# Kernel tuning notes

Measured on AMD Instinct MI355X. Metric: run time of the kernel, lower is better.

Reference implementation:

```python
import jax, jax.numpy as jnp
import numpy as np


def setup_inputs() -> dict:
    key = jax.random.key(0)
    k1, k2, k3 = jax.random.split(key, 3)
    B, T, S, D = 8, 2048, 2048, 512
    main_input = jax.random.normal(k1, (B, T, D), dtype=jnp.float32)
    attn_input = jax.random.normal(k2, (B, S, D), dtype=jnp.float32)
    # f_input is a torch Linear(D, D): y = x @ W_f.T + b_f
    W_f = jax.random.normal(k3, (D, D), dtype=jnp.float32) * (1.0 / np.sqrt(D))
    b_f = jnp.zeros((D,), dtype=jnp.float32)
    return {"main_input": main_input, "attn_input": attn_input, "W_f": W_f, "b_f": b_f}


def reference(main_input, attn_input, W_f, b_f):
    # keys: f_input applied to each attn word  [B,S,D]
    keys = jnp.einsum("bsd,ed->bse", attn_input, W_f) + b_f
    # scores[b,t,s] = keys[b,s,:] . main_input[b,t,:]
    scores = jnp.einsum("bse,bte->bts", keys, main_input)
    attn = jax.nn.softmax(scores, axis=-1)  # softmax over attn words S
    # weighted sum of RAW attn_input (values are unprojected)
    out = jnp.einsum("bts,bsd->btd", attn, attn_input)
    return out
```

## Files before the change

kernel.cpp:

```cpp
#include <hip/hip_runtime.h>
#include <math.h>

#define B_  8
#define T_  2048
#define S_  2048
#define D_  512

typedef _Float16 half8   __attribute__((ext_vector_type(8)));
typedef _Float16 half4_t __attribute__((ext_vector_type(4)));
typedef float    floatx4 __attribute__((ext_vector_type(4)));

__device__ __forceinline__ floatx4 mfma16(half8 a, half8 b, floatx4 c) {
  return __builtin_amdgcn_mfma_f32_16x16x32_f16(a, b, c, 0, 0, 0);
}

__device__ __forceinline__ void async16(void* lds, const void* g) {
  __builtin_amdgcn_global_load_lds(
      (const __attribute__((address_space(1))) void*)g,
      (__attribute__((address_space(3))) void*)lds, 16, 0, 0);
}

__device__ __forceinline__ void bar_lds() {
  __builtin_amdgcn_sched_barrier(0);
  asm volatile("s_waitcnt lgkmcnt(0)" ::: "memory");
  __builtin_amdgcn_s_barrier();
  __builtin_amdgcn_sched_barrier(0);
}

__global__ __launch_bounds__(256) void transpose_cast_kernel(
    const float* __restrict__ attn, _Float16* __restrict__ Vt) {
  __shared__ _Float16 tile[32][33];
  const int tx = threadIdx.x, ty = threadIdx.y;
  const int b = blockIdx.z, s0 = blockIdx.y * 32, d0 = blockIdx.x * 32;
  const float* src = attn + ((size_t)b * S_ + s0) * D_ + d0;
#pragma unroll
  for (int i = 0; i < 4; ++i) {
    int s = ty + i * 8;
    tile[tx][s] = (_Float16)src[(size_t)s * D_ + tx];
  }
  __syncthreads();
  _Float16* dst = Vt + ((size_t)b * D_ + d0) * S_ + s0;
#pragma unroll
  for (int i = 0; i < 4; ++i) {
    int d = ty + i * 8;
    dst[(size_t)d * S_ + tx] = tile[d][tx];
  }
}

__global__ __launch_bounds__(512, 2) void keys_gemm_kernel(
    const float* __restrict__ X, const float* __restrict__ W,
    const float* __restrict__ bias, _Float16* __restrict__ K16) {
  __shared__ alignas(16) _Float16 Xs[128][72];
  __shared__ alignas(16) _Float16 Ws[128][72];
  const int t = threadIdx.x;
  const int wave = t >> 6, lane = t & 63, q = lane >> 4, n = lane & 15;
  const int wm = wave >> 2, wn = wave & 3;
  const int m0 = blockIdx.x * 128, n0 = blockIdx.y * 128;

  floatx4 acc[4][2];
#pragma unroll
  for (int i = 0; i < 4; ++i)
#pragma unroll
    for (int j = 0; j < 2; ++j) {
      floatx4 z = {0.f, 0.f, 0.f, 0.f};
      acc[i][j] = z;
    }

  for (int kc = 0; kc < 8; ++kc) {
    const int k0 = kc * 64;
#pragma unroll
    for (int i = 0; i < 4; ++i) {
      int seg = i * 512 + t;
      int row = seg >> 4, c4 = (seg & 15) * 4;
      floatx4 xv = *(const floatx4*)&X[(size_t)(m0 + row) * D_ + k0 + c4];
      floatx4 wv = *(const floatx4*)&W[(size_t)(n0 + row) * D_ + k0 + c4];
      half4_t xh, wh;
#pragma unroll
      for (int j = 0; j < 4; ++j) { xh[j] = (_Float16)xv[j]; wh[j] = (_Float16)wv[j]; }
      *(half4_t*)&Xs[row][c4] = xh;
      *(half4_t*)&Ws[row][c4] = wh;
    }
    __syncthreads();
#pragma unroll
    for (int kk = 0; kk < 2; ++kk) {
      half8 a[4], bb[2];
#pragma unroll
      for (int mt = 0; mt < 4; ++mt)
        a[mt] = *(const half8*)&Xs[wm * 64 + mt * 16 + n][kk * 32 + q * 8];
#pragma unroll
      for (int nt = 0; nt < 2; ++nt)
        bb[nt] = *(const half8*)&Ws[wn * 32 + nt * 16 + n][kk * 32 + q * 8];
#pragma unroll
      for (int mt = 0; mt < 4; ++mt)
#pragma unroll
        for (int nt = 0; nt < 2; ++nt)
          acc[mt][nt] = mfma16(a[mt], bb[nt], acc[mt][nt]);
    }
    __syncthreads();
  }

#pragma unroll
  for (int nt = 0; nt < 2; ++nt) {
    int col = n0 + wn * 32 + nt * 16 + n;
    float bv = bias[col];
#pragma unroll
    for (int mt = 0; mt < 4; ++mt)
#pragma unroll
      for (int r = 0; r < 4; ++r) {
        int row = m0 + wm * 64 + mt * 16 + q * 4 + r;
        K16[(size_t)row * D_ + col] = (_Float16)(acc[mt][nt][r] + bv);
      }
  }
}

__global__ __launch_bounds__(512, 2) void flash_kernel(
    const float* __restrict__ Qf, const _Float16* __restrict__ K16,
    const _Float16* __restrict__ Vt, float* __restrict__ out) {
  __shared__ alignas(16) _Float16 Klds[2][32][512];
  __shared__ alignas(16) _Float16 Vlds[2][512][32];
  __shared__ alignas(16) _Float16 Pscr[4][16][40];
  __shared__ float Mscr[4][2][16];

  const int t = threadIdx.x;
  const int w = t >> 6, lane = t & 63, qd = lane >> 4, n = lane & 15;
  const int n7 = n & 7;
  const int rg = w >> 1, h = w & 1;
  const int bid = blockIdx.x;
  const int b = bid & 7, t0 = (bid >> 3) * 64;

  const _Float16* Kb = K16 + (size_t)b * S_ * D_;
  const _Float16* Vb = Vt + (size_t)b * D_ * S_;

  const int vsw = (lane & 3) ^ ((lane >> 3) & 3);
  const int ccV = qd ^ ((n >> 1) & 3);

  half8 qreg[16];
  {
    const float* qrow = Qf + ((size_t)b * T_ + t0 + rg * 16 + n) * D_;
#pragma unroll
    for (int kk = 0; kk < 16; ++kk) {
      floatx4 v0 = *(const floatx4*)&qrow[kk * 32 + qd * 8];
      floatx4 v1 = *(const floatx4*)&qrow[kk * 32 + qd * 8 + 4];
      half8 hv;
#pragma unroll
      for (int j = 0; j < 4; ++j) { hv[j] = (_Float16)v0[j]; hv[j + 4] = (_Float16)v1[j]; }
      qreg[kk] = hv;
    }
  }

  floatx4 O[17];
#pragma unroll
  for (int ng = 0; ng < 17; ++ng) {
    floatx4 z = {0.f, 0.f, 0.f, 0.f};
    O[ng] = z;
  }
  float m_st[4];
#pragma unroll
  for (int r = 0; r < 4; ++r) m_st[r] = -1e30f;

  half8 ones8;
#pragma unroll
  for (int j = 0; j < 8; ++j) ones8[j] = (_Float16)1.0f;

#pragma unroll
  for (int i = 0; i < 4; ++i) {
    int row = w * 4 + i;
    async16(&Klds[0][row][0], Kb + (size_t)row * D_ + ((lane ^ (row & 7)) * 8));
  }
#pragma unroll
  for (int i = 0; i < 4; ++i) {
    int d0 = (w * 4 + i) * 16;
    async16(&Vlds[0][d0][0], Vb + (size_t)(d0 + (lane >> 2)) * S_ + vsw * 8);
  }
  __syncthreads();

  for (int st = 0; st < S_ / 32; ++st) {
    const int cur = st & 1, nxt = cur ^ 1;
    const int s0 = st * 32;

    if (st < S_ / 32 - 1) {
#pragma unroll
      for (int i = 0; i < 4; ++i) {
        int row = w * 4 + i;
        async16(&Klds[nxt][row][0],
                Kb + (size_t)(s0 + 32 + row) * D_ + ((lane ^ (row & 7)) * 8));
      }
#pragma unroll
      for (int i = 0; i < 4; ++i) {
        int d0 = (w * 4 + i) * 16;
        async16(&Vlds[nxt][d0][0],
                Vb + (size_t)(d0 + (lane >> 2)) * S_ + s0 + 32 + vsw * 8);
      }
    }

    floatx4 Sa = {0.f, 0.f, 0.f, 0.f}, Sb = Sa;
#pragma unroll
    for (int kk = 0; kk < 8; ++kk) {
      int slot = (kk * 4 + qd) ^ n7;
      half8 bk = *(const half8*)&Klds[cur][h * 16 + n][slot * 8];
      Sa = mfma16(qreg[kk], bk, Sa);
    }
#pragma unroll
    for (int kk = 8; kk < 16; ++kk) {
      int slot = (kk * 4 + qd) ^ n7;
      half8 bk = *(const half8*)&Klds[cur][h * 16 + n][slot * 8];
      Sb = mfma16(qreg[kk], bk, Sb);
    }
    floatx4 Sc = Sa + Sb;

#pragma unroll
    for (int r = 0; r < 4; ++r) {
      float v = Sc[r];
      v = fmaxf(v, __shfl_xor(v, 1, 16));
      v = fmaxf(v, __shfl_xor(v, 2, 16));
      v = fmaxf(v, __shfl_xor(v, 4, 16));
      v = fmaxf(v, __shfl_xor(v, 8, 16));
      if (n == qd * 4 + r) Mscr[rg][h][n] = v;
    }
    bar_lds();

    float alpha[4];
#pragma unroll
    for (int r = 0; r < 4; ++r) {
      int row = qd * 4 + r;
      float mt = fmaxf(Mscr[rg][0][row], Mscr[rg][1][row]);
      float mn = fmaxf(m_st[r], mt);
      alpha[r] = __expf(m_st[r] - mn);
      m_st[r] = mn;
    }
    bool unchanged = (alpha[0] == 1.f) & (alpha[1] == 1.f) &
                     (alpha[2] == 1.f) & (alpha[3] == 1.f);
    if (!__all(unchanged)) {
#pragma unroll
      for (int ng = 0; ng < 17; ++ng)
#pragma unroll
        for (int r = 0; r < 4; ++r) O[ng][r] *= alpha[r];
    }

#pragma unroll
    for (int r = 0; r < 4; ++r) {
      float p = __expf(Sc[r] - m_st[r]);
      Pscr[rg][qd * 4 + r][h * 16 + n] = (_Float16)p;
    }
    bar_lds();

    half8 av = *(const half8*)&Pscr[rg][n][qd * 8];

#pragma unroll
    for (int ng = 0; ng < 16; ++ng) {
      half8 bv = *(const half8*)&Vlds[cur][h * 256 + ng * 16 + n][ccV * 8];
      O[ng] = mfma16(av, bv, O[ng]);
    }
    O[16] = mfma16(av, ones8, O[16]);

    if (st < S_ / 32 - 1) __syncthreads();
  }

  float* ob = out + ((size_t)b * T_ + t0 + rg * 16) * D_ + h * 256;
#pragma unroll
  for (int r = 0; r < 4; ++r) {
    float inv = 1.f / O[16][r];
    const size_t rowoff = (size_t)(qd * 4 + r) * D_;
#pragma unroll
    for (int ng = 0; ng < 16; ++ng)
      ob[rowoff + ng * 16 + n] = O[ng][r] * inv;
  }
}

extern "C" void kernel_launch(void* const* d_in, const int* in_sizes, int n_in,
                              void* d_out, int out_size, void* d_ws, size_t ws_size,
                              hipStream_t stream) {
  (void)in_sizes; (void)n_in; (void)out_size; (void)ws_size;
  const float* main_in = (const float*)d_in[0];
  const float* attn_in = (const float*)d_in[1];
  const float* W_f     = (const float*)d_in[2];
  const float* b_f     = (const float*)d_in[3];
  float* out = (float*)d_out;

  _Float16* K16 = (_Float16*)d_ws;
  _Float16* Vt  = K16 + (size_t)B_ * S_ * D_;

  transpose_cast_kernel<<<dim3(D_ / 32, S_ / 32, B_), dim3(32, 8, 1), 0, stream>>>(
      attn_in, Vt);
  keys_gemm_kernel<<<dim3((B_ * S_) / 128, D_ / 128), 512, 0, stream>>>(
      attn_in, W_f, b_f, K16);
  flash_kernel<<<(B_ * T_) / 64, 512, 0, stream>>>(main_in, K16, Vt, out);
}
```

Measured before the change: 293.5 us.

## Split KV tile across wave pair to drop per-step max exchange barriers

Each wave in a pair now owns half of every 32-wide S tile and keeps its own independent running max and sum over the full D=512 output, using 16x16x16 MFMAs on its 16 keys. This removes the two LDS barriers per step that were used to share row maxima and P between the two waves. The partial results are merged once at the end through shared memory. The cost is double the O accumulator registers (33 floatx4 instead of 17), which risks register spills or lower occupancy under launch_bounds(512,2), and twice as many narrower MFMAs for P·V.

```diff
diff --git a/kernel.cpp b/kernel.cpp
--- a/kernel.cpp
+++ b/kernel.cpp
@@ -13,18 +13,14 @@
 __device__ __forceinline__ floatx4 mfma16(half8 a, half8 b, floatx4 c) {
   return __builtin_amdgcn_mfma_f32_16x16x32_f16(a, b, c, 0, 0, 0);
 }
+__device__ __forceinline__ floatx4 mfma16k16(half4_t a, half4_t b, floatx4 c) {
+  return __builtin_amdgcn_mfma_f32_16x16x16f16(a, b, c, 0, 0, 0);
+}
 
 __device__ __forceinline__ void async16(void* lds, const void* g) {
   __builtin_amdgcn_global_load_lds(
       (const __attribute__((address_space(1))) void*)g,
       (__attribute__((address_space(3))) void*)lds, 16, 0, 0);
-}
-
-__device__ __forceinline__ void bar_lds() {
-  __builtin_amdgcn_sched_barrier(0);
-  asm volatile("s_waitcnt lgkmcnt(0)" ::: "memory");
-  __builtin_amdgcn_s_barrier();
-  __builtin_amdgcn_sched_barrier(0);
 }
 
 __global__ __launch_bounds__(256) void transpose_cast_kernel(
@@ -116,10 +112,11 @@
 __global__ __launch_bounds__(512, 2) void flash_kernel(
     const float* __restrict__ Qf, const _Float16* __restrict__ K16,
     const _Float16* __restrict__ Vt, float* __restrict__ out) {
-  __shared__ alignas(16) _Float16 Klds[2][32][512];
-  __shared__ alignas(16) _Float16 Vlds[2][512][32];
-  __shared__ alignas(16) _Float16 Pscr[4][16][40];
-  __shared__ float Mscr[4][2][16];
+  __shared__ alignas(16) unsigned char smem[137728];
+  _Float16* Kl = (_Float16*)smem;
+  _Float16* Vl = (_Float16*)(smem + 65536);
+  _Float16* Pp = (_Float16*)(smem + 131072);
+  float*    Mm = (float*)(smem + 137216);
 
   const int t = threadIdx.x;
   const int w = t >> 6, lane = t & 63, qd = lane >> 4, n = lane & 15;
@@ -132,7 +129,7 @@
   const _Float16* Vb = Vt + (size_t)b * D_ * S_;
 
   const int vsw = (lane & 3) ^ ((lane >> 3) & 3);
-  const int ccV = qd ^ ((n >> 1) & 3);
+  const int voff = (((h * 2 + (qd >> 1)) ^ ((n >> 1) & 3)) * 8) + (qd & 1) * 4;
 
   half8 qreg[16];
   {
@@ -148,9 +145,9 @@
     }
   }
 
-  floatx4 O[17];
-#pragma unroll
-  for (int ng = 0; ng < 17; ++ng) {
+  floatx4 O[33];
+#pragma unroll
+  for (int ng = 0; ng < 33; ++ng) {
     floatx4 z = {0.f, 0.f, 0.f, 0.f};
     O[ng] = z;
   }
@@ -158,19 +155,19 @@
 #pragma unroll
   for (int r = 0; r < 4; ++r) m_st[r] = -1e30f;
 
-  half8 ones8;
-#pragma unroll
-  for (int j = 0; j < 8; ++j) ones8[j] = (_Float16)1.0f;
+  half4_t ones4;
+#pragma unroll
+  for (int j = 0; j < 4; ++j) ones4[j] = (_Float16)1.0f;
 
 #pragma unroll
   for (int i = 0; i < 4; ++i) {
     int row = w * 4 + i;
-    async16(&Klds[0][row][0], Kb + (size_t)row * D_ + ((lane ^ (row & 7)) * 8));
+    async16(Kl + (size_t)row * 512, Kb + (size_t)row * D_ + ((lane ^ (row & 7)) * 8));
   }
 #pragma unroll
   for (int i = 0; i < 4; ++i) {
     int d0 = (w * 4 + i) * 16;
-    async16(&Vlds[0][d0][0], Vb + (size_t)(d0 + (lane >> 2)) * S_ + vsw * 8);
+    async16(Vl + (size_t)d0 * 32, Vb + (size_t)(d0 + (lane >> 2)) * S_ + vsw * 8);
   }
   __syncthreads();
 
@@ -182,32 +179,32 @@
 #pragma unroll
       for (int i = 0; i < 4; ++i) {
         int row = w * 4 + i;
-        async16(&Klds[nxt][row][0],
+        async16(Kl + ((size_t)nxt * 32 + row) * 512,
                 Kb + (size_t)(s0 + 32 + row) * D_ + ((lane ^ (row & 7)) * 8));
       }
 #pragma unroll
       for (int i = 0; i < 4; ++i) {
         int d0 = (w * 4 + i) * 16;
-        async16(&Vlds[nxt][d0][0],
+        async16(Vl + ((size_t)nxt * 512 + d0) * 32,
                 Vb + (size_t)(d0 + (lane >> 2)) * S_ + s0 + 32 + vsw * 8);
       }
     }
 
+    const _Float16* krow = Kl + ((size_t)cur * 32 + h * 16 + n) * 512;
     floatx4 Sa = {0.f, 0.f, 0.f, 0.f}, Sb = Sa;
 #pragma unroll
     for (int kk = 0; kk < 8; ++kk) {
       int slot = (kk * 4 + qd) ^ n7;
-      half8 bk = *(const half8*)&Klds[cur][h * 16 + n][slot * 8];
-      Sa = mfma16(qreg[kk], bk, Sa);
+      Sa = mfma16(qreg[kk], *(const half8*)&krow[slot * 8], Sa);
     }
 #pragma unroll
     for (int kk = 8; kk < 16; ++kk) {
       int slot = (kk * 4 + qd) ^ n7;
-      half8 bk = *(const half8*)&Klds[cur][h * 16 + n][slot * 8];
-      Sb = mfma16(qreg[kk], bk, Sb);
+      Sb = mfma16(qreg[kk], *(const half8*)&krow[slot * 8], Sb);
     }
     floatx4 Sc = Sa + Sb;
 
+    float alpha[4];
 #pragma unroll
     for (int r = 0; r < 4; ++r) {
       float v = Sc[r];
@@ -215,16 +212,7 @@
       v = fmaxf(v, __shfl_xor(v, 2, 16));
       v = fmaxf(v, __shfl_xor(v, 4, 16));
       v = fmaxf(v, __shfl_xor(v, 8, 16));
-      if (n == qd * 4 + r) Mscr[rg][h][n] = v;
-    }
-    bar_lds();
-
-    float alpha[4];
-#pragma unroll
-    for (int r = 0; r < 4; ++r) {
-      int row = qd * 4 + r;
-      float mt = fmaxf(Mscr[rg][0][row], Mscr[rg][1][row]);
-      float mn = fmaxf(m_st[r], mt);
+      float mn = fmaxf(m_st[r], v);
       alpha[r] = __expf(m_st[r] - mn);
       m_st[r] = mn;
     }
@@ -232,7 +220,7 @@
                      (alpha[2] == 1.f) & (alpha[3] == 1.f);
     if (!__all(unchanged)) {
 #pragma unroll
-      for (int ng = 0; ng < 17; ++ng)
+      for (int ng = 0; ng < 33; ++ng)
 #pragma unroll
         for (int r = 0; r < 4; ++r) O[ng][r] *= alpha[r];
     }
@@ -240,30 +228,64 @@
 #pragma unroll
     for (int r = 0; r < 4; ++r) {
       float p = __expf(Sc[r] - m_st[r]);
-      Pscr[rg][qd * 4 + r][h * 16 + n] = (_Float16)p;
-    }
-    bar_lds();
-
-    half8 av = *(const half8*)&Pscr[rg][n][qd * 8];
-
-#pragma unroll
-    for (int ng = 0; ng < 16; ++ng) {
-      half8 bv = *(const half8*)&Vlds[cur][h * 256 + ng * 16 + n][ccV * 8];
-      O[ng] = mfma16(av, bv, O[ng]);
-    }
-    O[16] = mfma16(av, ones8, O[16]);
+      Pp[((size_t)w * 16 + qd * 4 + r) * 24 + n] = (_Float16)p;
+    }
+    half4_t av = *(const half4_t*)&Pp[((size_t)w * 16 + n) * 24 + qd * 4];
+
+    const _Float16* vbase = Vl + (size_t)cur * 512 * 32;
+#pragma unroll
+    for (int ng = 0; ng < 32; ++ng) {
+      half4_t bv = *(const half4_t*)&vbase[(size_t)(ng * 16 + n) * 32 + voff];
+      O[ng] = mfma16k16(av, bv, O[ng]);
+    }
+    O[32] = mfma16k16(av, ones4, O[32]);
 
     if (st < S_ / 32 - 1) __syncthreads();
   }
 
-  float* ob = out + ((size_t)b * T_ + t0 + rg * 16) * D_ + h * 256;
+  if (n == 0) {
+#pragma unroll
+    for (int r = 0; r < 4; ++r) Mm[w * 16 + qd * 4 + r] = m_st[r];
+  }
+  __syncthreads();
+
+  float fac[4], lp[4];
 #pragma unroll
   for (int r = 0; r < 4; ++r) {
-    float inv = 1.f / O[16][r];
-    const size_t rowoff = (size_t)(qd * 4 + r) * D_;
-#pragma unroll
-    for (int ng = 0; ng < 16; ++ng)
-      ob[rowoff + ng * 16 + n] = O[ng][r] * inv;
+    float mo = Mm[(w ^ 1) * 16 + qd * 4 + r];
+    float mn = fmaxf(m_st[r], mo);
+    fac[r] = __expf(m_st[r] - mn);
+    lp[r] = O[32][r] * fac[r];
+  }
+
+  float* Ob = (float*)smem;
+  float* Lb = (float*)(smem + 131072);
+  if (h == 1) {
+#pragma unroll
+    for (int ng = 0; ng < 32; ++ng)
+#pragma unroll
+      for (int r = 0; r < 4; ++r)
+        Ob[(size_t)(rg * 16 + qd * 4 + r) * 512 + ng * 16 + n] = O[ng][r] * fac[r];
+    if (n == 0) {
+#pragma unroll
+      for (int r = 0; r < 4; ++r) Lb[rg * 16 + qd * 4 + r] = lp[r];
+    }
+  }
+  __syncthreads();
+
+  if (h == 0) {
+    float* ob = out + ((size_t)b * T_ + t0 + rg * 16) * D_;
+#pragma unroll
+    for (int r = 0; r < 4; ++r) {
+      float lt = lp[r] + Lb[rg * 16 + qd * 4 + r];
+      float inv = 1.f / lt;
+      const size_t rowoff = (size_t)(qd * 4 + r) * D_;
+#pragma unroll
+      for (int ng = 0; ng < 32; ++ng)
+        ob[rowoff + ng * 16 + n] =
+            (O[ng][r] * fac[r] +
+             Ob[(size_t)(rg * 16 + qd * 4 + r) * 512 + ng * 16 + n]) * inv;
+    }
   }
 }
 
```

Result: slower. 381.2 us (+29.9%).

## Precompute LDS/global byte offsets, interleave QK MFMAs, lazy softmax rescale, set priority

Applied to the files above, without the earlier changes.

Replaces per-iteration index arithmetic for the K/V async loads and LDS fragment reads with precomputed byte pointers and incremented offsets. It interleaves the two QK accumulator chains and wraps the MFMA loops in s_setprio to favour matrix issue. The online-softmax rescale now runs only when a row max grows by more than 8 (lazy rescaling). This lets exp values exceed 1 by up to e^8 in fp16, which adds some overflow and precision risk. The goal is fewer VALU/SALU instructions and skipped O rescales.

```diff
diff --git a/kernel.cpp b/kernel.cpp
--- a/kernel.cpp
+++ b/kernel.cpp
@@ -128,11 +128,29 @@
   const int bid = blockIdx.x;
   const int b = bid & 7, t0 = (bid >> 3) * 64;
 
-  const _Float16* Kb = K16 + (size_t)b * S_ * D_;
-  const _Float16* Vb = Vt + (size_t)b * D_ * S_;
+  const char* Kb = (const char*)(K16 + (size_t)b * S_ * D_);
+  const char* Vb = (const char*)(Vt + (size_t)b * D_ * S_);
 
   const int vsw = (lane & 3) ^ ((lane >> 3) & 3);
   const int ccV = qd ^ ((n >> 1) & 3);
+
+  const int ks = n7 >> 2;
+  const int kq = (qd ^ (n7 & 3)) * 16;
+  const int krow_b = (h * 16 + n) * 1024;
+  const char* KL = (const char*)Klds;
+  const char* kbe0 = KL + krow_b + kq + ks * 64;
+  const char* kbo0 = KL + krow_b + kq + 64 - ks * 64;
+  const char* VL = (const char*)Vlds;
+  const char* vb0 = VL + h * 16384 + n * 64 + ccV * 16;
+  const _Float16* prd = &Pscr[rg][n][qd * 8];
+
+  unsigned int koff[4], voff[4];
+#pragma unroll
+  for (int i = 0; i < 4; ++i) {
+    int row = w * 4 + i;
+    koff[i] = (unsigned int)((row * 512 + (lane ^ (row & 7)) * 8) * 2);
+    voff[i] = (unsigned int)(((row * 16 + (lane >> 2)) * S_ + vsw * 8) * 2);
+  }
 
   half8 qreg[16];
   {
@@ -165,47 +183,37 @@
 #pragma unroll
   for (int i = 0; i < 4; ++i) {
     int row = w * 4 + i;
-    async16(&Klds[0][row][0], Kb + (size_t)row * D_ + ((lane ^ (row & 7)) * 8));
-  }
-#pragma unroll
-  for (int i = 0; i < 4; ++i) {
-    int d0 = (w * 4 + i) * 16;
-    async16(&Vlds[0][d0][0], Vb + (size_t)(d0 + (lane >> 2)) * S_ + vsw * 8);
+    async16(&Klds[0][row][0], Kb + koff[i]);
+    async16(&Vlds[0][row * 16][0], Vb + voff[i]);
+    koff[i] += 32768;
+    voff[i] += 64;
   }
   __syncthreads();
 
   for (int st = 0; st < S_ / 32; ++st) {
     const int cur = st & 1, nxt = cur ^ 1;
-    const int s0 = st * 32;
 
     if (st < S_ / 32 - 1) {
 #pragma unroll
       for (int i = 0; i < 4; ++i) {
         int row = w * 4 + i;
-        async16(&Klds[nxt][row][0],
-                Kb + (size_t)(s0 + 32 + row) * D_ + ((lane ^ (row & 7)) * 8));
+        async16(&Klds[nxt][row][0], Kb + koff[i]);
+        async16(&Vlds[nxt][row * 16][0], Vb + voff[i]);
+        koff[i] += 32768;
+        voff[i] += 64;
       }
-#pragma unroll
-      for (int i = 0; i < 4; ++i) {
-        int d0 = (w * 4 + i) * 16;
-        async16(&Vlds[nxt][d0][0],
-                Vb + (size_t)(d0 + (lane >> 2)) * S_ + s0 + 32 + vsw * 8);
-      }
-    }
-
+    }
+
+    const char* ke = (cur ? kbe0 + 32768 : kbe0);
+    const char* ko = (cur ? kbo0 + 32768 : kbo0);
     floatx4 Sa = {0.f, 0.f, 0.f, 0.f}, Sb = Sa;
-#pragma unroll
-    for (int kk = 0; kk < 8; ++kk) {
-      int slot = (kk * 4 + qd) ^ n7;
-      half8 bk = *(const half8*)&Klds[cur][h * 16 + n][slot * 8];
-      Sa = mfma16(qreg[kk], bk, Sa);
-    }
-#pragma unroll
-    for (int kk = 8; kk < 16; ++kk) {
-      int slot = (kk * 4 + qd) ^ n7;
-      half8 bk = *(const half8*)&Klds[cur][h * 16 + n][slot * 8];
-      Sb = mfma16(qreg[kk], bk, Sb);
-    }
+    __builtin_amdgcn_s_setprio(1);
+#pragma unroll
+    for (int j = 0; j < 8; ++j) {
+      Sa = mfma16(qreg[2 * j],     *(const half8*)(ke + j * 128), Sa);
+      Sb = mfma16(qreg[2 * j + 1], *(const half8*)(ko + j * 128), Sb);
+    }
+    __builtin_amdgcn_s_setprio(0);
     floatx4 Sc = Sa + Sb;
 
 #pragma unroll
@@ -219,22 +227,22 @@
     }
     bar_lds();
 
-    float alpha[4];
+    float pm[4], need = 0.f;
 #pragma unroll
     for (int r = 0; r < 4; ++r) {
       int row = qd * 4 + r;
-      float mt = fmaxf(Mscr[rg][0][row], Mscr[rg][1][row]);
-      float mn = fmaxf(m_st[r], mt);
-      alpha[r] = __expf(m_st[r] - mn);
-      m_st[r] = mn;
-    }
-    bool unchanged = (alpha[0] == 1.f) & (alpha[1] == 1.f) &
-                     (alpha[2] == 1.f) & (alpha[3] == 1.f);
-    if (!__all(unchanged)) {
-#pragma unroll
-      for (int ng = 0; ng < 17; ++ng)
-#pragma unroll
-        for (int r = 0; r < 4; ++r) O[ng][r] *= alpha[r];
+      pm[r] = fmaxf(Mscr[rg][0][row], Mscr[rg][1][row]);
+      need = fmaxf(need, pm[r] - m_st[r]);
+    }
+    if (__any(need > 8.f)) {
+#pragma unroll
+      for (int r = 0; r < 4; ++r) {
+        float mn = fmaxf(m_st[r], pm[r]);
+        float al = __expf(m_st[r] - mn);
+        m_st[r] = mn;
+#pragma unroll
+        for (int ng = 0; ng < 17; ++ng) O[ng][r] *= al;
+      }
     }
 
 #pragma unroll
@@ -244,14 +252,16 @@
     }
     bar_lds();
 
-    half8 av = *(const half8*)&Pscr[rg][n][qd * 8];
-
+    half8 av = *(const half8*)prd;
+
+    const char* vbp = (cur ? vb0 + 32768 : vb0);
+    __builtin_amdgcn_s_setprio(1);
 #pragma unroll
     for (int ng = 0; ng < 16; ++ng) {
-      half8 bv = *(const half8*)&Vlds[cur][h * 256 + ng * 16 + n][ccV * 8];
-      O[ng] = mfma16(av, bv, O[ng]);
+      O[ng] = mfma16(av, *(const half8*)(vbp + ng * 1024), O[ng]);
     }
     O[16] = mfma16(av, ones8, O[16]);
+    __builtin_amdgcn_s_setprio(0);
 
     if (st < S_ / 32 - 1) __syncthreads();
   }
```

Measured after the change: 311.7 us. 6.2% more time.
